# Performance work log

Measured on AMD Instinct MI355X. Metric: run time of the kernel, lower is better.

Reference implementation:

```python
import jax, jax.numpy as jnp
import numpy as np

SIZE_MIN, SIZE_MAX = 10.0, 40.0
CROP = 28


def convert_to_box_list(x):
    # [B, C, W, H] -> [W*H, B, C]
    b, c, w, h = x.shape
    return jnp.transpose(x, (2, 3, 0, 1)).reshape(w * h, b, c)


def invert_convert_to_box_list(x, w, h):
    # [W*H, B, C] -> [B, C, W, H]
    n, b, c = x.shape
    return jnp.transpose(x.reshape(w, h, b, c), (2, 3, 0, 1))


def bilinear_sample(img, x, y):
    # img: [C, W, H]; x, y: pixel coords of shape S -> [C, *S]; zero outside.
    C, W, H = img.shape
    x0 = jnp.floor(x); y0 = jnp.floor(y)
    x1 = x0 + 1.0; y1 = y0 + 1.0
    wx1 = x - x0; wx0 = 1.0 - wx1
    wy1 = y - y0; wy0 = 1.0 - wy1
    def fetch(xi, yi):
        valid = ((xi >= 0) & (xi < W) & (yi >= 0) & (yi < H)).astype(img.dtype)
        xc = jnp.clip(xi, 0, W - 1).astype(jnp.int32)
        yc = jnp.clip(yi, 0, H - 1).astype(jnp.int32)
        return img[:, xc, yc] * valid
    return (fetch(x0, y0) * (wx0 * wy0) + fetch(x1, y0) * (wx1 * wy0)
            + fetch(x0, y1) * (wx0 * wy1) + fetch(x1, y1) * (wx1 * wy1))


def crop(bx, by, bw, bh, big, ws, hs):
    # bx..bh: [k, B]; big: [B, C, W, H] -> [k, B, C, ws, hs]
    u = (jnp.arange(ws) + 0.5) / ws
    v = (jnp.arange(hs) + 0.5) / hs
    xs = bx[..., None] - 0.5 * bw[..., None] + u * bw[..., None] - 0.5  # [k,B,ws]
    ys = by[..., None] - 0.5 * bh[..., None] + v * bh[..., None] - 0.5  # [k,B,hs]
    def one(xr, yr, img):
        X = jnp.broadcast_to(xr[:, None], (ws, hs))
        Y = jnp.broadcast_to(yr[None, :], (ws, hs))
        return bilinear_sample(img, X, Y)
    return jax.vmap(jax.vmap(one, (0, 0, 0)), (0, 0, None))(xs, ys, big)


def uncrop(bx, by, bw, bh, small, Wb, Hb):
    # small: [k, B, C, ws, hs] -> [k, B, C, Wb, Hb] (zero outside each box)
    ws, hs = small.shape[-2], small.shape[-1]
    Xc = jnp.arange(Wb) + 0.5
    Yc = jnp.arange(Hb) + 0.5
    xs = (Xc - (bx[..., None] - 0.5 * bw[..., None])) / bw[..., None] * ws - 0.5
    ys = (Yc - (by[..., None] - 0.5 * bh[..., None])) / bh[..., None] * hs - 0.5
    def one(xr, yr, img):
        X = jnp.broadcast_to(xr[:, None], (Wb, Hb))
        Y = jnp.broadcast_to(yr[None, :], (Wb, Hb))
        return bilinear_sample(img, X, Y)
    return jax.vmap(jax.vmap(one, (0, 0, 0)), (0, 0, 0))(xs, ys, small)


def tmaps_to_bb(tmaps, W_raw, H_raw):
    # tmaps: [B, 4, nw, nh] in (0,1) -> box lists [n_all, B]
    nw, nh = tmaps.shape[-2], tmaps.shape[-1]
    tx, ty, tw, th = tmaps[:, 0], tmaps[:, 1], tmaps[:, 2], tmaps[:, 3]
    ix = jnp.arange(nw, dtype=tmaps.dtype)[:, None]
    iy = jnp.arange(nh, dtype=tmaps.dtype)[None, :]
    bx_map = W_raw * (ix + tx) / nw
    by_map = H_raw * (iy + ty) / nh
    bw_map = SIZE_MIN + (SIZE_MAX - SIZE_MIN) * tw
    bh_map = SIZE_MIN + (SIZE_MAX - SIZE_MIN) * th
    tolist = lambda m: convert_to_box_list(m[:, None]).squeeze(-1)
    return tolist(bx_map), tolist(by_map), tolist(bw_map), tolist(bh_map)


def forward_core(logit_mu, zwhere_mu, zwhere_std, eps_zwhere, eps_zinstance,
                 features, w_zwhere, b_zwhere, w_enc, b_enc, w_dec, b_dec, n_objects_max):
    B, Cf, W_raw, H_raw = features.shape
    nw, nh = logit_mu.shape[-2], logit_mu.shape[-1]

    # zwhere posterior sample + KL vs N(0,1)
    zwhere_sample_map = zwhere_mu + zwhere_std * eps_zwhere
    zwhere_kl_map = 0.5 * (zwhere_mu ** 2 + zwhere_std ** 2) - jnp.log(zwhere_std) - 0.5

    # decode zwhere (1x1 conv) -> sigmoid tmaps -> boxes
    tmaps = jax.nn.sigmoid(jnp.einsum('bzwh,cz->bcwh', zwhere_sample_map, w_zwhere)
                           + b_zwhere[None, :, None, None])
    bx_all, by_all, bw_all, bh_all = tmaps_to_bb(tmaps, W_raw, H_raw)

    area_all = bw_all * bh_all
    area_map = invert_convert_to_box_list(area_all[..., None], nw, nh)

    # c sample = logit map (deterministic relaxation of the DPP/Bernoulli sample)
    c_sample_map = logit_mu
    prob_map = jax.nn.sigmoid(c_sample_map)
    c_all = convert_to_box_list(c_sample_map).squeeze(-1)   # [n_all, B]
    prob_all = convert_to_box_list(prob_map).squeeze(-1)

    # top-k per batch element (indices constant wrt grads)
    k = min(n_objects_max, c_all.shape[0])
    idx = jax.lax.stop_gradient(jax.lax.top_k(c_all.T, k)[1].T)  # [k, B]
    take = lambda t: jnp.take_along_axis(t, idx, axis=0)
    c_few, prob_few = take(c_all), take(prob_all)
    bx_few, by_few, bw_few, bh_few = take(bx_all), take(by_all), take(bw_all), take(bh_all)

    zwhere_sample_all = convert_to_box_list(zwhere_sample_map)  # [n_all, B, Z]
    zwhere_kl_all = convert_to_box_list(zwhere_kl_map)
    idx_z = idx[..., None]
    zwhere_sample_few = jnp.take_along_axis(zwhere_sample_all, idx_z, axis=0)
    zwhere_kl_few = jnp.take_along_axis(zwhere_kl_all, idx_z, axis=0)

    # crop full-res features at the k boxes -> [k, B, Cf, CROP, CROP]
    cropped = crop(bx_few, by_few, bw_few, bh_few, features, CROP, CROP)

    # encoder zinstance (flatten + linear -> mu, std)
    flat = cropped.reshape(k, B, -1)
    enc = jnp.einsum('kbf,df->kbd', flat, w_enc) + b_enc
    dim_z = enc.shape[-1] // 2
    zi_mu = enc[..., :dim_z]
    zi_std = jax.nn.softplus(enc[..., dim_z:]) + 1e-4
    zi_sample = zi_mu + zi_std * eps_zinstance
    zi_kl = 0.5 * (zi_mu ** 2 + zi_std ** 2) - jnp.log(zi_std) - 0.5

    # decoder zinstance (linear -> [k, B, 2, CROP, CROP])
    dec = jnp.einsum('kbz,fz->kbf', zi_sample, w_dec) + b_dec
    raw = dec.reshape(k, B, 2, CROP, CROP)
    small = jnp.concatenate([jax.nn.softplus(raw[..., :1, :, :]),
                             jax.nn.sigmoid(raw[..., 1:, :, :])], axis=-3)

    big_stuff = uncrop(bx_few, by_few, bw_few, bh_few,
                       small * c_few[..., None, None, None], W_raw, H_raw)
    big_weight = big_stuff[..., :1, :, :]
    big_img = big_stuff[..., 1:, :, :]

    # from_weights_to_masks over box dim (dim=-5 of [k,B,1,W,H])
    sum_w = jnp.sum(big_weight, axis=0, keepdims=True)
    big_mask = jnp.tanh(sum_w) * (big_weight / jnp.maximum(sum_w, 1e-6))
    big_mask_non = jnp.tanh(big_weight)

    return (prob_map, area_map, c_few, prob_few, bx_few, by_few, bw_few, bh_few,
            big_mask, big_mask_non, big_img,
            zwhere_sample_few, zwhere_kl_few, zi_sample, zi_kl)


def setup_inputs() -> dict:
    key = jax.random.key(0)
    ks = jax.random.split(key, 9)
    B, NW, NH = 8, 32, 32
    W_RAW = H_RAW = 128
    CF, ZW, ZI, K = 32, 8, 32, 48
    fan_in = CF * CROP * CROP
    return {
        "logit_mu": jax.random.normal(ks[0], (B, 1, NW, NH), jnp.float32),
        "zwhere_mu": 0.5 * jax.random.normal(ks[1], (B, ZW, NW, NH), jnp.float32),
        "zwhere_std": jax.random.uniform(ks[2], (B, ZW, NW, NH), jnp.float32, 0.1, 1.0),
        "eps_zwhere": jax.random.normal(ks[3], (B, ZW, NW, NH), jnp.float32),
        "eps_zinstance": jax.random.normal(ks[4], (K, B, ZI), jnp.float32),
        "features": jax.random.normal(ks[5], (B, CF, W_RAW, H_RAW), jnp.float32),
        "w_zwhere": 0.3 * jax.random.normal(ks[6], (4, ZW), jnp.float32),
        "b_zwhere": jnp.zeros((4,), jnp.float32),
        "w_enc": jax.random.normal(ks[7], (2 * ZI, fan_in), jnp.float32) / np.sqrt(fan_in).astype(np.float32),
        "b_enc": jnp.zeros((2 * ZI,), jnp.float32),
        "w_dec": jax.random.normal(ks[8], (2 * CROP * CROP, ZI), jnp.float32) / np.sqrt(ZI).astype(np.float32),
        "b_dec": jnp.zeros((2 * CROP * CROP,), jnp.float32),
        "n_objects_max": 48,
    }


def reference(logit_mu, zwhere_mu, zwhere_std, eps_zwhere, eps_zinstance, features,
              w_zwhere, b_zwhere, w_enc, b_enc, w_dec, b_dec, n_objects_max):
    return forward_core(logit_mu, zwhere_mu, zwhere_std, eps_zwhere, eps_zinstance,
                        features, w_zwhere, b_zwhere, w_enc, b_enc, w_dec, b_dec,
                        n_objects_max)
```

## Files before the change

kernel.cpp:

```cpp
#include <hip/hip_runtime.h>
#include <math.h>

#define B 8
#define NWD 32
#define NHD 32
#define NBOX 1024
#define ZWD 8
#define ZID 32
#define KOBJ 48
#define CFEAT 32
#define WRAW 128
#define HRAW 128
#define CR 28
#define CR2 784
#define FAN 25088
#define KB 384

#define OFF_PROB   0
#define OFF_AREA   8192
#define OFF_CFEW   16384
#define OFF_PFEW   16768
#define OFF_BXF    17152
#define OFF_BYF    17536
#define OFF_BWF    17920
#define OFF_BHF    18304
#define OFF_BMASK  18688
#define OFF_BMASKN 6310144
#define OFF_BIMG   12601600
#define OFF_ZWS    18893056
#define OFF_ZWK    18896128
#define OFF_ZIS    18899200
#define OFF_ZIK    18911488

#define WS_SMALL 32768

#define SCR_PART 0
#define SCR_WT   1204224

#define FSPLIT 49
#define FPB 512
#define CHK 128
#define NCH 4
#define MKB 16
#define KSTR 152
#define TAPN (MKB*28)

typedef __attribute__((ext_vector_type(8))) short bfrag;
typedef __attribute__((ext_vector_type(4))) float f32x4;

__device__ __forceinline__ float sigm(float x){ return 1.0f/(1.0f+expf(-x)); }
__device__ __forceinline__ float softpl(float x){ return fmaxf(x,0.0f) + log1pf(expf(-fabsf(x))); }
__device__ __forceinline__ float ftanh(float x){
  float t = __expf(2.0f*x);
  return 1.0f - __fdividef(2.0f, t + 1.0f);
}
__device__ __forceinline__ unsigned short f2bf(float f){
  unsigned u = __float_as_uint(f);
  unsigned r = u + 0x7FFFu + ((u >> 16) & 1u);
  return (unsigned short)(r >> 16);
}
__device__ __forceinline__ unsigned okey(float f){
  unsigned b = __float_as_uint(f);
  return b ^ ((b & 0x80000000u) ? 0xFFFFFFFFu : 0x80000000u);
}

__global__ __launch_bounds__(256) void prep_kernel(
    const float* __restrict__ wenc, unsigned short* __restrict__ wt,
    const float* __restrict__ logit, const float* __restrict__ zmu,
    const float* __restrict__ zstd, const float* __restrict__ zeps,
    const float* __restrict__ wz, const float* __restrict__ bz,
    float* __restrict__ out){
  __shared__ __align__(16) unsigned su[NBOX];
  if (blockIdx.x < 784){
    const int ks = blockIdx.x;
    const int tid = threadIdx.x;
    const int lane = tid & 63;
    const int t = tid >> 6;
    const int d = t*16 + (lane & 15);
    const int k0 = ks*32 + (lane >> 4)*8;
    const float* src = wenc + (size_t)d*FAN + k0;
    float4 a = *(const float4*)src;
    float4 b = *(const float4*)(src + 4);
    unsigned long long p0 = (unsigned long long)f2bf(a.x)
      | ((unsigned long long)f2bf(a.y) << 16)
      | ((unsigned long long)f2bf(a.z) << 32)
      | ((unsigned long long)f2bf(a.w) << 48);
    unsigned long long p1 = (unsigned long long)f2bf(b.x)
      | ((unsigned long long)f2bf(b.y) << 16)
      | ((unsigned long long)f2bf(b.z) << 32)
      | ((unsigned long long)f2bf(b.w) << 48);
    unsigned short* dst = wt + ((size_t)ks*256 + tid)*8;
    *(unsigned long long*)dst       = p0;
    *(unsigned long long*)(dst + 4) = p1;
    return;
  }
  const int bid = blockIdx.x - 784;
  const int b  = bid >> 2;
  const int sb = bid & 3;
  const int tid = threadIdx.x;
  #pragma unroll
  for (int u = 0; u < 4; u++){
    int j = tid + u*256;
    su[j] = okey(logit[b*NBOX + j]);
  }
  const int n = sb*256 + tid;
  const int w = n >> 5, h = n & 31;
  float acc0=bz[0], acc1=bz[1], acc2=bz[2], acc3=bz[3];
  #pragma unroll
  for(int z=0; z<ZWD; z++){
    int id = ((b*ZWD + z)*NWD + w)*NHD + h;
    float s = zmu[id] + zstd[id]*zeps[id];
    acc0 += s*wz[0*ZWD+z]; acc1 += s*wz[1*ZWD+z];
    acc2 += s*wz[2*ZWD+z]; acc3 += s*wz[3*ZWD+z];
  }
  float tx=sigm(acc0), ty=sigm(acc1), tw=sigm(acc2), th=sigm(acc3);
  float bx = (128.0f*((float)w + tx))/32.0f;
  float by = (128.0f*((float)h + ty))/32.0f;
  float bwv = 10.0f + 30.0f*tw;
  float bhv = 10.0f + 30.0f*th;
  float lg = logit[b*NBOX + n];
  out[OFF_PROB + b*NBOX + n] = sigm(lg);
  out[OFF_AREA + b*NBOX + n] = bwv*bhv;
  __syncthreads();
  const unsigned ui = su[n];
  const uint4* su4 = (const uint4*)su;
  int rank = 0;
  #pragma unroll 4
  for (int jq = 0; jq < NBOX/4; jq++){
    uint4 v = su4[jq];
    int j = jq*4;
    rank += (v.x > ui || (v.x == ui && j   < n)) ? 1 : 0;
    rank += (v.y > ui || (v.y == ui && j+1 < n)) ? 1 : 0;
    rank += (v.z > ui || (v.z == ui && j+2 < n)) ? 1 : 0;
    rank += (v.w > ui || (v.w == ui && j+3 < n)) ? 1 : 0;
  }
  if (rank < KOBJ){
    out[OFF_CFEW + rank*B + b] = lg;
    out[OFF_PFEW + rank*B + b] = sigm(lg);
    out[OFF_BXF  + rank*B + b] = bx;
    out[OFF_BYF  + rank*B + b] = by;
    out[OFF_BWF  + rank*B + b] = bwv;
    out[OFF_BHF  + rank*B + b] = bhv;
    #pragma unroll
    for(int z=0; z<ZWD; z++){
      int id = ((b*ZWD + z)*NWD + w)*NHD + h;
      float mu = zmu[id], sd = zstd[id];
      out[OFF_ZWS + (rank*B+b)*ZWD + z] = mu + sd*zeps[id];
      out[OFF_ZWK + (rank*B+b)*ZWD + z] = 0.5f*(mu*mu + sd*sd) - logf(sd) - 0.5f;
    }
  }
}

__global__ __launch_bounds__(256, 4) void enc_kernel(
    const float* __restrict__ feat, const unsigned short* __restrict__ wt,
    const float* __restrict__ outc, float* __restrict__ part){
  __shared__ __align__(16) unsigned short cl0[MKB*KSTR];
  __shared__ __align__(16) unsigned short cl1[MKB*KSTR];
  __shared__ float2 wxs[TAPN]; __shared__ int2 xos[TAPN];
  __shared__ float2 wys[TAPN]; __shared__ int2 yos[TAPN];
  __shared__ float rAx[MKB], rSx[MKB], rAy[MKB], rSy[MKB];
  const int tid = threadIdx.x;
  const int fs  = blockIdx.x % FSPLIT;
  const int kb0 = (blockIdx.x / FSPLIT) * MKB;
  if (tid < MKB){
    float bx = outc[OFF_BXF + kb0 + tid];
    float by = outc[OFF_BYF + kb0 + tid];
    float bw = outc[OFF_BWF + kb0 + tid];
    float bh = outc[OFF_BHF + kb0 + tid];
    float sx = bw * (1.0f/(float)CR), sy = bh * (1.0f/(float)CR);
    rSx[tid] = sx; rSy[tid] = sy;
    rAx[tid] = bx - 0.5f*bw + 0.5f*sx - 0.5f;
    rAy[tid] = by - 0.5f*bh + 0.5f*sy - 0.5f;
  }
  __syncthreads();
  #pragma unroll
  for (int it = 0; it < 4; it++){
    int idx = it*256 + tid;
    if (idx < 2*TAPN){
      int isy = idx >= TAPN;
      int q = idx - (isy ? TAPN : 0);
      int rr = q / 28, i = q - rr*28;
      float A = isy ? rAy[rr] : rAx[rr];
      float S = isy ? rSy[rr] : rSx[rr];
      float x = fmaf((float)i, S, A);
      float x0f = floorf(x); int x0 = (int)x0f;
      float w1 = x - x0f, w0 = 1.0f - w1;
      if ((unsigned)x0     >= WRAW) w0 = 0.f;
      if ((unsigned)(x0+1) >= WRAW) w1 = 0.f;
      int c0 = min(max(x0,0),WRAW-1), c1 = min(max(x0+1,0),WRAW-1);
      if (isy){ wys[q] = make_float2(w0,w1); yos[q] = make_int2(c0, c1); }
      else    { wxs[q] = make_float2(w0,w1); xos[q] = make_int2(c0*HRAW, c1*HRAW); }
    }
  }
  __syncthreads();
  float raw[8][4];
  int ji[8];
  const int fblk = fs*FPB;
  #define GATHER(CH) { \
    _Pragma("unroll") \
    for (int u = 0; u < 8; u++){ \
      int idx = u*256 + tid; \
      int rr = idx >> 7, ff = idx & 127; \
      int f = fblk + (CH)*CHK + ff; \
      int c = f / CR2; int p = f - c*CR2; \
      int i = p / CR;  int j = p - i*CR; \
      int ii = rr*28 + i, jj = rr*28 + j; \
      ji[u] = (jj << 16) | ii; \
      int2 xo = xos[ii]; int2 yo = yos[jj]; \
      const float* img = feat + (size_t)((rr & (B-1))*CFEAT + c)*(WRAW*HRAW); \
      raw[u][0] = img[xo.x + yo.x]; \
      raw[u][1] = img[xo.x + yo.y]; \
      raw[u][2] = img[xo.y + yo.x]; \
      raw[u][3] = img[xo.y + yo.y]; \
    } }
  #define STORE(DST) { \
    _Pragma("unroll") \
    for (int u = 0; u < 8; u++){ \
      int idx = u*256 + tid; \
      int rr = idx >> 7, ff = idx & 127; \
      int ii = ji[u] & 0xffff, jj = ji[u] >> 16; \
      float2 wx = wxs[ii]; float2 wy = wys[jj]; \
      float v = (raw[u][0]*wy.x + raw[u][1]*wy.y)*wx.x \
              + (raw[u][2]*wy.x + raw[u][3]*wy.y)*wx.y; \
      (DST)[rr*KSTR + ff] = f2bf(v); \
    } }
  GATHER(0);
  STORE(cl0);
  __syncthreads();
  const int lane = tid & 63, wv = tid >> 6;
  const int lr = lane & 15, lg = lane >> 4;
  f32x4 acc = {0.f,0.f,0.f,0.f};
  #pragma unroll
  for (int ch = 0; ch < NCH; ch++){
    unsigned short* cur = (ch & 1) ? cl1 : cl0;
    unsigned short* nxt = (ch & 1) ? cl0 : cl1;
    const unsigned short* bptr = wt + (size_t)(fs*16 + ch*4)*2048 + wv*512 + lane*8;
    bfrag b0 = *(const bfrag*)(bptr);
    bfrag b1 = *(const bfrag*)(bptr + 2048);
    bfrag b2 = *(const bfrag*)(bptr + 4096);
    bfrag b3 = *(const bfrag*)(bptr + 6144);
    if (ch < NCH-1){ GATHER(ch+1); }
    const unsigned short* arow = &cur[lr*KSTR + lg*8];
    bfrag a0 = *(const bfrag*)(arow);
    bfrag a1 = *(const bfrag*)(arow + 32);
    bfrag a2 = *(const bfrag*)(arow + 64);
    bfrag a3 = *(const bfrag*)(arow + 96);
    acc = __builtin_amdgcn_mfma_f32_16x16x32_bf16(a0, b0, acc, 0, 0, 0);
    acc = __builtin_amdgcn_mfma_f32_16x16x32_bf16(a1, b1, acc, 0, 0, 0);
    acc = __builtin_amdgcn_mfma_f32_16x16x32_bf16(a2, b2, acc, 0, 0, 0);
    acc = __builtin_amdgcn_mfma_f32_16x16x32_bf16(a3, b3, acc, 0, 0, 0);
    if (ch < NCH-1){ STORE(nxt); }
    __syncthreads();
  }
  float* dst = part + ((size_t)fs*KB + kb0)*64;
  #pragma unroll
  for (int r = 0; r < 4; r++){
    int row = lg*4 + r;
    dst[row*64 + wv*16 + lr] = acc[r];
  }
  #undef GATHER
  #undef STORE
}

__global__ __launch_bounds__(256) void zi_dec_kernel(
    const float* __restrict__ part, const float* __restrict__ benc,
    const float* __restrict__ ieps, const float* __restrict__ wdec,
    const float* __restrict__ bdec, float* __restrict__ out,
    float* __restrict__ ws){
  int kb = blockIdx.x;
  int d = threadIdx.x & 63, seg = threadIdx.x >> 6;
  float s0=0.f, s1=0.f;
  for (int f = seg; f < FSPLIT; f += 8)
    s0 += part[((size_t)f*KB + kb)*64 + d];
  for (int f = seg+4; f < FSPLIT; f += 8)
    s1 += part[((size_t)f*KB + kb)*64 + d];
  __shared__ float red[4][64];
  __shared__ float zs[ZID];
  __shared__ float cf_s;
  red[seg][d] = s0 + s1;
  __syncthreads();
  if (threadIdx.x < ZID){
    int dd = threadIdx.x;
    float mu = benc[dd]     + red[0][dd]     + red[1][dd]     + red[2][dd]     + red[3][dd];
    float pe = benc[ZID+dd] + red[0][ZID+dd] + red[1][ZID+dd] + red[2][ZID+dd] + red[3][ZID+dd];
    float sd = softpl(pe) + 1e-4f;
    float zsv = mu + sd*ieps[kb*ZID + dd];
    out[OFF_ZIS + kb*ZID + dd] = zsv;
    out[OFF_ZIK + kb*ZID + dd] = 0.5f*(mu*mu + sd*sd) - logf(sd) - 0.5f;
    zs[dd] = zsv;
  }
  if (threadIdx.x == 0) cf_s = out[OFF_CFEW + kb];
  __syncthreads();
  float cf = cf_s;
  for (int f = threadIdx.x; f < 2*CR2; f += 256){
    float a = bdec[f];
    #pragma unroll
    for (int q = 0; q < 8; q++){
      float4 w4 = *(const float4*)&wdec[f*ZID + q*4];
      a = fmaf(zs[q*4+0], w4.x, a);
      a = fmaf(zs[q*4+1], w4.y, a);
      a = fmaf(zs[q*4+2], w4.z, a);
      a = fmaf(zs[q*4+3], w4.w, a);
    }
    float v = (f < CR2) ? softpl(a) : sigm(a);
    ws[WS_SMALL + (size_t)kb*(2*CR2) + f] = v*cf;
  }
}

__global__ __launch_bounds__(256) void uncrop_compose_kernel(
    const float* __restrict__ ws, float* __restrict__ out){
  const int t = blockIdx.x*256 + threadIdx.x;
  const int b = t >> 14, p = t & 16383;
  const int X = p >> 7, Y = p & 127;
  __shared__ float sAx[KOBJ], sSx[KOBJ], sAy[KOBJ], sSy[KOBJ];
  if (threadIdx.x < KOBJ){
    int k = threadIdx.x;
    float bx = out[OFF_BXF + k*B + b], bw = out[OFF_BWF + k*B + b];
    float by = out[OFF_BYF + k*B + b], bh = out[OFF_BHF + k*B + b];
    float ix = __fdividef((float)CR, bw), iy = __fdividef((float)CR, bh);
    sSx[k] = ix; sAx[k] = (0.5f*bw - bx)*ix - 0.5f;
    sSy[k] = iy; sAy[k] = (0.5f*bh - by)*iy - 0.5f;
  }
  __syncthreads();
  const float xc = (float)X + 0.5f, yc = (float)Y + 0.5f;
  float wr[KOBJ];
  float vi[KOBJ];
  float sum = 0.f;
  #pragma unroll
  for (int k = 0; k < KOBJ; k++){
    float x = fmaf(xc, sSx[k], sAx[k]);
    float v0 = 0.f, v1 = 0.f;
    if (x > -1.0f && x < (float)CR){
      float y = fmaf(yc, sSy[k], sAy[k]);
      const float* sm = ws + WS_SMALL + (size_t)(k*B + b)*(2*CR2);
      float x0f = floorf(x), y0f = floorf(y);
      int x0 = (int)x0f, y0 = (int)y0f;
      float wx1 = x - x0f, wx0 = 1.0f - wx1;
      float wy1 = y - y0f, wy0 = 1.0f - wy1;
      if ((unsigned)x0     >= CR) wx0 = 0.f;
      if ((unsigned)(x0+1) >= CR) wx1 = 0.f;
      if ((unsigned)y0     >= CR) wy0 = 0.f;
      if ((unsigned)(y0+1) >= CR) wy1 = 0.f;
      int x0c = min(max(x0,0),CR-1), x1c = min(max(x0+1,0),CR-1);
      int y0c = min(max(y0,0),CR-1), y1c = min(max(y0+1,0),CR-1);
      const float* r0 = sm + x0c*CR;
      const float* r1 = sm + x1c*CR;
      v0 = (r0[y0c]*wy0 + r0[y1c]*wy1)*wx0 + (r1[y0c]*wy0 + r1[y1c]*wy1)*wx1;
      const float* q0 = r0 + CR2;
      const float* q1 = r1 + CR2;
      v1 = (q0[y0c]*wy0 + q0[y1c]*wy1)*wx0 + (q1[y0c]*wy0 + q1[y1c]*wy1)*wx1;
    }
    wr[k] = v0; vi[k] = v1; sum += v0;
  }
  #pragma unroll
  for (int k = 0; k < KOBJ; k++)
    out[OFF_BIMG + (size_t)(k*B + b)*16384 + p] = vi[k];
  float th = ftanh(sum);
  float inv = 1.0f / fmaxf(sum, 1e-6f);
  #pragma unroll
  for (int k = 0; k < KOBJ; k++){
    size_t o = (size_t)(k*B + b)*16384 + p;
    out[OFF_BMASK  + o] = th * (wr[k] * inv);
    out[OFF_BMASKN + o] = (wr[k] == 0.f) ? 0.f : ftanh(wr[k]);
  }
}

extern "C" void kernel_launch(void* const* d_in, const int* in_sizes, int n_in,
                              void* d_out, int out_size, void* d_ws, size_t ws_size,
                              hipStream_t stream) {
  (void)in_sizes; (void)n_in; (void)out_size; (void)ws_size;
  const float* logit = (const float*)d_in[0];
  const float* zmu   = (const float*)d_in[1];
  const float* zstd  = (const float*)d_in[2];
  const float* zeps  = (const float*)d_in[3];
  const float* ieps  = (const float*)d_in[4];
  const float* feat  = (const float*)d_in[5];
  const float* wz    = (const float*)d_in[6];
  const float* bz    = (const float*)d_in[7];
  const float* wenc  = (const float*)d_in[8];
  const float* benc  = (const float*)d_in[9];
  const float* wdec  = (const float*)d_in[10];
  const float* bdec  = (const float*)d_in[11];
  float* out = (float*)d_out;
  float* ws  = (float*)d_ws;
  float* scr = out + OFF_BMASK;
  float* part = scr + SCR_PART;
  unsigned short* wt = (unsigned short*)(scr + SCR_WT);

  prep_kernel         <<<784 + B*4, 256, 0, stream>>>(wenc, wt, logit, zmu, zstd, zeps, wz, bz, out);
  enc_kernel          <<<(KB/MKB)*FSPLIT, 256, 0, stream>>>(feat, wt, out, part);
  zi_dec_kernel       <<<KB, 256, 0, stream>>>(part, benc, ieps, wdec, bdec, out, ws);
  uncrop_compose_kernel<<<(B*WRAW*HRAW)/256, 256, 0, stream>>>(ws, out);
}
```

Baseline: 91.61 us.

## Transpose features to channel-last and reorder encoder K dimension for vectorized gathers

The prep kernel now also writes a channel-last copy of the feature map into scratch, and the encoder weights are repacked in a pixel-major K order. The encoder gather then reads 8 contiguous channels per bilinear tap with float4 loads, where it previously issued scalar loads from separate channel planes. Each thread packs 8 bf16 values into shared memory with 64-bit stores. The cost is an extra transpose pass over the features and strided, uncoalesced reads of the encoder weights during repacking.

New measurement: 103.0 us. 1.12x slower.

```diff
diff --git a/kernel.cpp b/kernel.cpp
--- a/kernel.cpp
+++ b/kernel.cpp
@@ -36,9 +36,9 @@
 
 #define SCR_PART 0
 #define SCR_WT   1204224
+#define SCR_FT   2007040
 
 #define FSPLIT 49
-#define FPB 512
 #define CHK 128
 #define NCH 4
 #define MKB 16
@@ -66,38 +66,55 @@
 
 __global__ __launch_bounds__(256) void prep_kernel(
     const float* __restrict__ wenc, unsigned short* __restrict__ wt,
+    const float* __restrict__ feat, float* __restrict__ featT,
     const float* __restrict__ logit, const float* __restrict__ zmu,
     const float* __restrict__ zstd, const float* __restrict__ zeps,
     const float* __restrict__ wz, const float* __restrict__ bz,
     float* __restrict__ out){
-  __shared__ __align__(16) unsigned su[NBOX];
+  __shared__ __align__(16) float lsh[32*129];
+  const int tid = threadIdx.x;
   if (blockIdx.x < 784){
     const int ks = blockIdx.x;
-    const int tid = threadIdx.x;
     const int lane = tid & 63;
     const int t = tid >> 6;
     const int d = t*16 + (lane & 15);
-    const int k0 = ks*32 + (lane >> 4)*8;
-    const float* src = wenc + (size_t)d*FAN + k0;
-    float4 a = *(const float4*)src;
-    float4 b = *(const float4*)(src + 4);
-    unsigned long long p0 = (unsigned long long)f2bf(a.x)
-      | ((unsigned long long)f2bf(a.y) << 16)
-      | ((unsigned long long)f2bf(a.z) << 32)
-      | ((unsigned long long)f2bf(a.w) << 48);
-    unsigned long long p1 = (unsigned long long)f2bf(b.x)
-      | ((unsigned long long)f2bf(b.y) << 16)
-      | ((unsigned long long)f2bf(b.z) << 32)
-      | ((unsigned long long)f2bf(b.w) << 48);
+    const int c0 = (lane >> 4)*8;
+    const float* src = wenc + (size_t)d*FAN + ks;
+    unsigned long long p0 = 0ull, p1 = 0ull;
+    #pragma unroll
+    for (int e = 0; e < 4; e++)
+      p0 |= (unsigned long long)f2bf(src[(size_t)(c0+e)*CR2]) << (16*e);
+    #pragma unroll
+    for (int e = 0; e < 4; e++)
+      p1 |= (unsigned long long)f2bf(src[(size_t)(c0+4+e)*CR2]) << (16*e);
     unsigned short* dst = wt + ((size_t)ks*256 + tid)*8;
     *(unsigned long long*)dst       = p0;
     *(unsigned long long*)(dst + 4) = p1;
     return;
   }
-  const int bid = blockIdx.x - 784;
+  if (blockIdx.x < 1808){
+    const int bid = blockIdx.x - 784;
+    const int b = bid >> 7, X = bid & 127;
+    #pragma unroll
+    for (int u = 0; u < 16; u++){
+      int idx = u*256 + tid;
+      int c = idx >> 7, Y = idx & 127;
+      lsh[c*129 + Y] = feat[(((size_t)b*CFEAT + c)*WRAW + X)*HRAW + Y];
+    }
+    __syncthreads();
+    float* dstrow = featT + ((size_t)b*16384 + (size_t)X*128)*32;
+    #pragma unroll
+    for (int u = 0; u < 16; u++){
+      int idx = u*256 + tid;
+      int Y = idx >> 5, c = idx & 31;
+      dstrow[Y*32 + c] = lsh[c*129 + Y];
+    }
+    return;
+  }
+  const int bid = blockIdx.x - 1808;
   const int b  = bid >> 2;
   const int sb = bid & 3;
-  const int tid = threadIdx.x;
+  unsigned* su = (unsigned*)lsh;
   #pragma unroll
   for (int u = 0; u < 4; u++){
     int j = tid + u*256;
@@ -152,7 +169,7 @@
 }
 
 __global__ __launch_bounds__(256, 4) void enc_kernel(
-    const float* __restrict__ feat, const unsigned short* __restrict__ wt,
+    const float* __restrict__ featT, const unsigned short* __restrict__ wt,
     const float* __restrict__ outc, float* __restrict__ part){
   __shared__ __align__(16) unsigned short cl0[MKB*KSTR];
   __shared__ __align__(16) unsigned short cl1[MKB*KSTR];
@@ -193,37 +210,50 @@
     }
   }
   __syncthreads();
-  float raw[8][4];
-  int ji[8];
-  const int fblk = fs*FPB;
+  const int grr = tid >> 4;
+  const int gpq = (tid >> 2) & 3;
+  const int gcg = tid & 3;
+  const float* gbase = featT + ((size_t)(grr & (B-1))*16384)*32 + gcg*8;
+  const int gkk = gpq*32 + gcg*8;
+  float4 t00a, t00b, t01a, t01b, t10a, t10b, t11a, t11b;
+  float2 gwx, gwy;
   #define GATHER(CH) { \
+    int pos = fs*16 + (CH)*4 + gpq; \
+    int i = pos / 28, j = pos - i*28; \
+    int ii = grr*28 + i, jj = grr*28 + j; \
+    gwx = wxs[ii]; gwy = wys[jj]; \
+    int2 xo = xos[ii]; int2 yo = yos[jj]; \
+    const float* p00 = gbase + (size_t)(xo.x + yo.x)*32; \
+    const float* p01 = gbase + (size_t)(xo.x + yo.y)*32; \
+    const float* p10 = gbase + (size_t)(xo.y + yo.x)*32; \
+    const float* p11 = gbase + (size_t)(xo.y + yo.y)*32; \
+    t00a = *(const float4*)p00; t00b = *(const float4*)(p00+4); \
+    t01a = *(const float4*)p01; t01b = *(const float4*)(p01+4); \
+    t10a = *(const float4*)p10; t10b = *(const float4*)(p10+4); \
+    t11a = *(const float4*)p11; t11b = *(const float4*)(p11+4); \
+  }
+  #define STORE(DST) { \
+    float s[8]; \
+    const float* q00 = (const float*)&t00a; const float* q01 = (const float*)&t01a; \
+    const float* q10 = (const float*)&t10a; const float* q11 = (const float*)&t11a; \
     _Pragma("unroll") \
-    for (int u = 0; u < 8; u++){ \
-      int idx = u*256 + tid; \
-      int rr = idx >> 7, ff = idx & 127; \
-      int f = fblk + (CH)*CHK + ff; \
-      int c = f / CR2; int p = f - c*CR2; \
-      int i = p / CR;  int j = p - i*CR; \
-      int ii = rr*28 + i, jj = rr*28 + j; \
-      ji[u] = (jj << 16) | ii; \
-      int2 xo = xos[ii]; int2 yo = yos[jj]; \
-      const float* img = feat + (size_t)((rr & (B-1))*CFEAT + c)*(WRAW*HRAW); \
-      raw[u][0] = img[xo.x + yo.x]; \
-      raw[u][1] = img[xo.x + yo.y]; \
-      raw[u][2] = img[xo.y + yo.x]; \
-      raw[u][3] = img[xo.y + yo.y]; \
-    } }
-  #define STORE(DST) { \
+    for (int e = 0; e < 4; e++) \
+      s[e] = (q00[e]*gwy.x + q01[e]*gwy.y)*gwx.x + (q10[e]*gwy.x + q11[e]*gwy.y)*gwx.y; \
+    q00 = (const float*)&t00b; q01 = (const float*)&t01b; \
+    q10 = (const float*)&t10b; q11 = (const float*)&t11b; \
     _Pragma("unroll") \
-    for (int u = 0; u < 8; u++){ \
-      int idx = u*256 + tid; \
-      int rr = idx >> 7, ff = idx & 127; \
-      int ii = ji[u] & 0xffff, jj = ji[u] >> 16; \
-      float2 wx = wxs[ii]; float2 wy = wys[jj]; \
-      float v = (raw[u][0]*wy.x + raw[u][1]*wy.y)*wx.x \
-              + (raw[u][2]*wy.x + raw[u][3]*wy.y)*wx.y; \
-      (DST)[rr*KSTR + ff] = f2bf(v); \
-    } }
+    for (int e = 0; e < 4; e++) \
+      s[4+e] = (q00[e]*gwy.x + q01[e]*gwy.y)*gwx.x + (q10[e]*gwy.x + q11[e]*gwy.y)*gwx.y; \
+    unsigned long long pk0 = 0ull, pk1 = 0ull; \
+    _Pragma("unroll") \
+    for (int e = 0; e < 4; e++){ \
+      pk0 |= (unsigned long long)f2bf(s[e])   << (16*e); \
+      pk1 |= (unsigned long long)f2bf(s[4+e]) << (16*e); \
+    } \
+    unsigned short* dp = &(DST)[grr*KSTR + gkk]; \
+    *(unsigned long long*)dp       = pk0; \
+    *(unsigned long long*)(dp + 4) = pk1; \
+  }
   GATHER(0);
   STORE(cl0);
   __syncthreads();
@@ -386,9 +416,11 @@
   float* scr = out + OFF_BMASK;
   float* part = scr + SCR_PART;
   unsigned short* wt = (unsigned short*)(scr + SCR_WT);
-
-  prep_kernel         <<<784 + B*4, 256, 0, stream>>>(wenc, wt, logit, zmu, zstd, zeps, wz, bz, out);
-  enc_kernel          <<<(KB/MKB)*FSPLIT, 256, 0, stream>>>(feat, wt, out, part);
+  float* featT = scr + SCR_FT;
+
+  prep_kernel         <<<784 + 1024 + B*4, 256, 0, stream>>>(wenc, wt, feat, featT,
+                                                             logit, zmu, zstd, zeps, wz, bz, out);
+  enc_kernel          <<<(KB/MKB)*FSPLIT, 256, 0, stream>>>(featT, wt, out, part);
   zi_dec_kernel       <<<KB, 256, 0, stream>>>(part, benc, ieps, wdec, bdec, out, ws);
   uncrop_compose_kernel<<<(B*WRAW*HRAW)/256, 256, 0, stream>>>(ws, out);
 }
```
